# Optimization experiments

Hardware: AMD Instinct MI355X
Metric: run time of the kernel (lower is better)

## Reference

```python
import jax, jax.numpy as jnp
import numpy as np

B, S, D, V = 4, 1024, 512, 32000
INNER, NHM, DHM, QB = 1024, 4, 256, 4   # mLSTM: proj_factor 2.0 -> inner=2*D, 4 heads
NHS, DHS, K = 4, 128, 3                  # sLSTM: 4 heads over D, causal conv k=3
EPS = 1e-5


def layernorm(x, w):
    mu = x.mean(-1, keepdims=True)
    var = ((x - mu) ** 2).mean(-1, keepdims=True)
    return (x - mu) * jax.lax.rsqrt(var + EPS) * w


def headnorm(x, w):
    # x: (B,S,NH,DH) normalize per head over DH (GroupNorm), scale by w (NH*DH,)
    mu = x.mean(-1, keepdims=True)
    var = ((x - mu) ** 2).mean(-1, keepdims=True)
    xn = (x - mu) * jax.lax.rsqrt(var + EPS)
    b, s, nh, dh = x.shape
    return xn.reshape(b, s, nh * dh) * w


def causal_conv(x, w, bias):
    # depthwise causal conv: x (B,S,C), kernel w (C,K)
    k = w.shape[1]
    s = x.shape[1]
    xp = jnp.pad(x, ((0, 0), (k - 1, 0), (0, 0)))
    y = sum(xp[:, i:i + s, :] * w[:, i] for i in range(k))
    return y + bias


def blockdiag(x, w):
    # LinearHeadwiseExpand: block-diagonal linear, w (NB, out_bs, in_bs)
    b, s, _ = x.shape
    nb, ob, ib = w.shape
    return jnp.einsum('bsni,noi->bsno', x.reshape(b, s, nb, ib), w).reshape(b, s, nb * ob)


def mlstm_parallel(q, k, v, ig, fg):
    # parallel_stabilized_simple; q,k,v (B,NH,S,DH), ig/fg (B,NH,S)
    dh = q.shape[-1]
    s = q.shape[2]
    lf = jax.nn.log_sigmoid(fg)
    cs = jnp.cumsum(lf, axis=-1)
    logfmat = cs[..., :, None] - cs[..., None, :]      # (i,j) = sum_{j+1..i} log f
    mask = jnp.tril(jnp.ones((s, s), dtype=bool))
    logD = jnp.where(mask, logfmat + ig[..., None, :], -jnp.inf)
    maxD = logD.max(-1, keepdims=True)                 # rowwise stabilizer
    Dm = jnp.exp(logD - maxD)
    C = jnp.einsum('bhid,bhjd->bhij', q, k) * (dh ** -0.5) * Dm
    norm = jnp.maximum(jnp.abs(C.sum(-1, keepdims=True)), jnp.exp(-maxD))
    return jnp.einsum('bhij,bhjd->bhid', C / (norm + 1e-6), v)


def mlstm_block(x, p):
    (ln, Wup, convW, convb, Wq, Wk, Wv, Wi, bi, Wf, bf, skip, onorm, Wdown) = p
    b, s, _ = x.shape
    xin = layernorm(x, ln) @ Wup                        # (B,S,2*INNER)
    xm, z = jnp.split(xin, 2, axis=-1)
    xc = jax.nn.silu(causal_conv(xm, convW, convb))
    q = blockdiag(xc, Wq)
    kk = blockdiag(xc, Wk)
    v = blockdiag(xm, Wv)
    qkv = jnp.concatenate([q, kk, v], axis=-1)
    ig = (qkv @ Wi + bi).transpose(0, 2, 1)             # (B,NH,S)
    fg = (qkv @ Wf + bf).transpose(0, 2, 1)
    qh = q.reshape(b, s, NHM, DHM).transpose(0, 2, 1, 3)
    kh = kk.reshape(b, s, NHM, DHM).transpose(0, 2, 1, 3)
    vh = v.reshape(b, s, NHM, DHM).transpose(0, 2, 1, 3)
    h = mlstm_parallel(qh, kh, vh, ig, fg)              # (B,NH,S,DH)
    h = headnorm(h.transpose(0, 2, 1, 3), onorm)        # (B,S,INNER)
    h = (h + skip * xc) * jax.nn.silu(z)
    return x + h @ Wdown


def slstm_block(x, p):
    (ln1, convW, convb, Wig, Wfg, Wzg, Wog, R, bias, gn, ln2, Wu, Wd) = p
    b, s, _ = x.shape
    xn = layernorm(x, ln1)
    xc = jax.nn.silu(causal_conv(xn, convW, convb))

    def gate(inp, W):  # headwise linear, W (NH, DH, DH)
        return jnp.einsum('bshi,hoi->bsho', inp.reshape(b, s, NHS, DHS), W)

    # gate preactivations, gate order i,f,z,o: (B,S,4,NH,DH)
    Wx = jnp.stack([gate(xc, Wig), gate(xc, Wfg), gate(xn, Wzg), gate(xn, Wog)], axis=2)

    def step(carry, wx):
        y, c, n, m = carry
        raw = wx + jnp.einsum('bhd,hdge->bghe', y, R) + bias
        ir, fr, zr, orr = raw[:, 0], raw[:, 1], raw[:, 2], raw[:, 3]
        lfm = m + jax.nn.log_sigmoid(fr)
        mn = jnp.maximum(ir, lfm)                        # exp-gating stabilizer
        igt = jnp.exp(ir - mn)
        fgt = jnp.exp(lfm - mn)
        cn = fgt * c + igt * jnp.tanh(zr)
        nn_ = fgt * n + igt
        yn = jax.nn.sigmoid(orr) * cn / nn_
        return (yn, cn, nn_, mn), yn

    z0 = jnp.zeros((b, NHS, DHS), x.dtype)
    _, ys = jax.lax.scan(step, (z0, z0, z0, z0), Wx.transpose(1, 0, 2, 3, 4))
    h = x + headnorm(ys.transpose(1, 0, 2, 3), gn)
    # gated feedforward (proj_factor=1.0, gelu)
    u = layernorm(h, ln2) @ Wu
    g, up = jnp.split(u, 2, axis=-1)
    return h + (jax.nn.gelu(g, approximate=False) * up) @ Wd


def forward(x, emb, m0, s1, m2, post_ln, clf_W, clf_b):
    h = emb[x]
    h = mlstm_block(h, m0)
    h = slstm_block(h, s1)
    h = mlstm_block(h, m2)
    h = layernorm(h, post_ln)
    return h[:, -1, :] @ clf_W + clf_b


def setup_inputs() -> dict:
    key = jax.random.key(0)
    ks = iter(jax.random.split(key, 64))

    def rn(shape, s=0.02):
        return jax.random.normal(next(ks), shape, jnp.float32) * s

    def mblock():
        return dict(
            ln=jnp.ones((D,)), Wup=rn((D, 2 * INNER)),
            convW=rn((INNER, K), 0.1), convb=jnp.zeros((INNER,)),
            Wq=rn((INNER // QB, QB, QB), 0.2), Wk=rn((INNER // QB, QB, QB), 0.2),
            Wv=rn((INNER // QB, QB, QB), 0.2),
            Wi=rn((3 * INNER, NHM)), bi=rn((NHM,), 0.1),
            Wf=rn((3 * INNER, NHM)), bf=jnp.linspace(3.0, 6.0, NHM),
            skip=jnp.ones((INNER,)), onorm=jnp.ones((INNER,)), Wdown=rn((INNER, D)))

    m0 = mblock()
    m2 = mblock()
    emb = rn((V, D), 1.0).at[0].set(0.0)  # padding_idx=0 row zeroed
    inp = {'x': jax.random.randint(next(ks), (B, S), 0, V), 'emb': emb}
    for pre, m in (('m0_', m0), ('m2_', m2)):
        for k_, v_ in m.items():
            inp[pre + k_] = v_
    zb = jnp.zeros((NHS, DHS))
    inp.update(
        s1_ln1=jnp.ones((D,)), s1_convW=rn((D, K), 0.1), s1_convb=jnp.zeros((D,)),
        s1_Wig=rn((NHS, DHS, DHS), 0.1), s1_Wfg=rn((NHS, DHS, DHS), 0.1),
        s1_Wzg=rn((NHS, DHS, DHS), 0.1), s1_Wog=rn((NHS, DHS, DHS), 0.1),
        s1_R=rn((NHS, DHS, 4, DHS), 0.05),
        s1_b=jnp.stack([zb, jnp.linspace(3.0, 6.0, NHS)[:, None] * jnp.ones((NHS, DHS)), zb, zb], axis=0),
        s1_gn=jnp.ones((D,)), s1_ln2=jnp.ones((D,)),
        s1_Wu=rn((D, 2 * D)), s1_Wd=rn((D, D)),
        post_ln=jnp.ones((D,)), clf_W=rn((D, 1)), clf_b=jnp.zeros((1,)))
    return inp


def reference(x, emb, m0_ln, m0_Wup, m0_convW, m0_convb, m0_Wq, m0_Wk, m0_Wv, m0_Wi, m0_bi, m0_Wf, m0_bf, m0_skip, m0_onorm, m0_Wdown,
              s1_ln1, s1_convW, s1_convb, s1_Wig, s1_Wfg, s1_Wzg, s1_Wog, s1_R, s1_b, s1_gn, s1_ln2, s1_Wu, s1_Wd,
              m2_ln, m2_Wup, m2_convW, m2_convb, m2_Wq, m2_Wk, m2_Wv, m2_Wi, m2_bi, m2_Wf, m2_bf, m2_skip, m2_onorm, m2_Wdown,
              post_ln, clf_W, clf_b):
    m0 = (m0_ln, m0_Wup, m0_convW, m0_convb, m0_Wq, m0_Wk, m0_Wv, m0_Wi, m0_bi, m0_Wf, m0_bf, m0_skip, m0_onorm, m0_Wdown)
    s1 = (s1_ln1, s1_convW, s1_convb, s1_Wig, s1_Wfg, s1_Wzg, s1_Wog, s1_R, s1_b, s1_gn, s1_ln2, s1_Wu, s1_Wd)
    m2 = (m2_ln, m2_Wup, m2_convW, m2_convb, m2_Wq, m2_Wk, m2_Wv, m2_Wi, m2_bi, m2_Wf, m2_bf, m2_skip, m2_onorm, m2_Wdown)
    return forward(x, emb, m0, s1, m2, post_ln, clf_W, clf_b)
```

## Files before the change

### kernel.cpp

```cpp
#include <hip/hip_runtime.h>
#include <cstddef>
#include <cstdint>

#define EPSV 1e-5f

typedef __attribute__((ext_vector_type(8))) short bf16x8;
typedef __attribute__((ext_vector_type(4))) float f32x4;

__device__ __forceinline__ short f2bf(float f) {
  union { float f; unsigned u; } v; v.f = f;
  unsigned r = (v.u + 0x7FFFu + ((v.u >> 16) & 1u)) >> 16;
  return (short)r;
}
__device__ __forceinline__ float bf2f(short s) {
  union { unsigned u; float f; } v; v.u = ((unsigned)(unsigned short)s) << 16;
  return v.f;
}

__device__ __forceinline__ float wsum(float v) {
  v += __shfl_xor(v, 32, 64);
  v += __shfl_xor(v, 16, 64);
  v += __shfl_xor(v, 8, 64);
  v += __shfl_xor(v, 4, 64);
  v += __shfl_xor(v, 2, 64);
  v += __shfl_xor(v, 1, 64);
  return v;
}

__global__ __launch_bounds__(128) void k_embed(const int* __restrict__ x,
                                               const float* __restrict__ emb,
                                               float* __restrict__ out) {
  int t = blockIdx.x, tid = threadIdx.x;
  int row = x[t];
  const float4 v = *reinterpret_cast<const float4*>(emb + (size_t)row * 512 + tid * 4);
  *reinterpret_cast<float4*>(out + (size_t)t * 512 + tid * 4) = v;
}

__global__ __launch_bounds__(128) void k_ln512(const float* __restrict__ in,
                                               const float* __restrict__ w,
                                               float* __restrict__ outf,
                                               short* __restrict__ out16) {
  int t = blockIdx.x, tid = threadIdx.x;
  const float4 v = *reinterpret_cast<const float4*>(in + (size_t)t * 512 + tid * 4);
  float s = v.x + v.y + v.z + v.w;
  float s2 = v.x * v.x + v.y * v.y + v.z * v.z + v.w * v.w;
  s = wsum(s); s2 = wsum(s2);
  __shared__ float l1[2], l2[2];
  int wv = tid >> 6;
  if ((tid & 63) == 0) { l1[wv] = s; l2[wv] = s2; }
  __syncthreads();
  s = l1[0] + l1[1]; s2 = l2[0] + l2[1];
  float mu = s * (1.f / 512.f);
  float var = s2 * (1.f / 512.f) - mu * mu;
  float r = rsqrtf(var + EPSV);
  const float4 w4 = *reinterpret_cast<const float4*>(w + tid * 4);
  float4 o;
  o.x = (v.x - mu) * r * w4.x;
  o.y = (v.y - mu) * r * w4.y;
  o.z = (v.z - mu) * r * w4.z;
  o.w = (v.w - mu) * r * w4.w;
  if (outf) *reinterpret_cast<float4*>(outf + (size_t)t * 512 + tid * 4) = o;
  *reinterpret_cast<short4*>(out16 + (size_t)t * 512 + tid * 4) =
      make_short4(f2bf(o.x), f2bf(o.y), f2bf(o.z), f2bf(o.w));
}

template <bool OUT16, bool RES>
__global__ __launch_bounds__(256) void k_mm(
    const short* __restrict__ A, size_t sA1, size_t sA2, int lda,
    const short* __restrict__ B, size_t sB1, size_t sB2, int ldb,
    const float* __restrict__ Res, size_t sR1, size_t sR2, int ldr,
    void* __restrict__ Cv, size_t sC1, size_t sC2, int ldc,
    int K, int HB) {
  const int z = blockIdx.z, zh = z / HB, zl = z - zh * HB;
  A += zh * sA1 + zl * sA2;
  B += zh * sB1 + zl * sB2;
  const int bm = blockIdx.y * 128, bn = blockIdx.x * 128;
  const int tid = threadIdx.x, lane = tid & 63, w = tid >> 6;
  const int wr = w >> 1, wc = w & 1;
  const int l15 = lane & 15, l4 = lane >> 4;
  __shared__ short As[128 * 72];
  __shared__ short Bs[128 * 72];
  f32x4 acc[4][4];
#pragma unroll
  for (int i = 0; i < 4; ++i)
#pragma unroll
    for (int j = 0; j < 4; ++j) acc[i][j] = (f32x4){0.f, 0.f, 0.f, 0.f};
  const int srow = tid >> 3, sg = tid & 7;
  for (int k0 = 0; k0 < K; k0 += 64) {
    int4 ra[4], rb[4];
#pragma unroll
    for (int it = 0; it < 4; ++it) {
      int row = it * 32 + srow;
      ra[it] = *reinterpret_cast<const int4*>(A + (size_t)(bm + row) * lda + k0 + sg * 8);
      rb[it] = *reinterpret_cast<const int4*>(B + (size_t)(bn + row) * ldb + k0 + sg * 8);
    }
    __syncthreads();
#pragma unroll
    for (int it = 0; it < 4; ++it) {
      int row = it * 32 + srow;
      *reinterpret_cast<int4*>(As + row * 72 + sg * 8) = ra[it];
      *reinterpret_cast<int4*>(Bs + row * 72 + sg * 8) = rb[it];
    }
    __syncthreads();
#pragma unroll
    for (int kk = 0; kk < 2; ++kk) {
      bf16x8 af[4], bfr[4];
#pragma unroll
      for (int i = 0; i < 4; ++i) {
        af[i]  = *reinterpret_cast<const bf16x8*>(As + (wr * 64 + i * 16 + l15) * 72 + kk * 32 + l4 * 8);
        bfr[i] = *reinterpret_cast<const bf16x8*>(Bs + (wc * 64 + i * 16 + l15) * 72 + kk * 32 + l4 * 8);
      }
#pragma unroll
      for (int i = 0; i < 4; ++i)
#pragma unroll
        for (int j = 0; j < 4; ++j)
          acc[i][j] = __builtin_amdgcn_mfma_f32_16x16x32_bf16(af[i], bfr[j], acc[i][j], 0, 0, 0);
    }
  }
  const int row0 = bm + wr * 64 + l4 * 4, col0 = bn + wc * 64 + l15;
  if constexpr (OUT16) {
    short* C = (short*)Cv + zh * sC1 + zl * sC2;
#pragma unroll
    for (int mi = 0; mi < 4; ++mi)
#pragma unroll
      for (int r = 0; r < 4; ++r) {
        size_t ro = (size_t)(row0 + mi * 16 + r) * ldc;
#pragma unroll
        for (int ni = 0; ni < 4; ++ni) C[ro + col0 + ni * 16] = f2bf(acc[mi][ni][r]);
      }
  } else {
    float* C = (float*)Cv + zh * sC1 + zl * sC2;
    const float* Rp = Res ? (Res + zh * sR1 + zl * sR2) : nullptr;
#pragma unroll
    for (int mi = 0; mi < 4; ++mi)
#pragma unroll
      for (int r = 0; r < 4; ++r) {
        int rw = row0 + mi * 16 + r;
#pragma unroll
        for (int ni = 0; ni < 4; ++ni) {
          float vv = acc[mi][ni][r];
          if constexpr (RES) vv += Rp[(size_t)rw * ldr + col0 + ni * 16];
          C[(size_t)rw * ldc + col0 + ni * 16] = vv;
        }
      }
  }
}

__global__ __launch_bounds__(256) void k_transp(const float* __restrict__ in, size_t sI1, size_t sI2, int ldi,
                                                short* __restrict__ out, size_t sO1, size_t sO2, int ldo,
                                                int HB) {
  __shared__ float t[32][33];
  int z = blockIdx.z, zh = z / HB, zl = z - zh * HB;
  in += zh * sI1 + zl * sI2;
  out += zh * sO1 + zl * sO2;
  int r0 = blockIdx.x * 32, c0 = blockIdx.y * 32;
  int tx = threadIdx.x & 31, ty = threadIdx.x >> 5;
#pragma unroll
  for (int i = 0; i < 4; ++i) {
    int rr = ty + i * 8;
    t[rr][tx] = in[(size_t)(r0 + rr) * ldi + c0 + tx];
  }
  __syncthreads();
#pragma unroll
  for (int i = 0; i < 4; ++i) {
    int cr = ty + i * 8;
    out[(size_t)(c0 + cr) * ldo + r0 + tx] = f2bf(t[tx][cr]);
  }
}

__global__ __launch_bounds__(256) void k_conv_silu(const float* __restrict__ in, int inLd, int logC,
                                                   const float* __restrict__ w,
                                                   const float* __restrict__ bias,
                                                   float* __restrict__ out,
                                                   short* __restrict__ out16) {
  int idx = blockIdx.x * 256 + threadIdx.x;
  int C = 1 << logC;
  int t = idx >> logC, c = idx & (C - 1);
  int s = t & 1023;
  const float* ip = in + (size_t)t * inLd + c;
  float acc = bias[c] + w[c * 3 + 2] * ip[0];
  if (s >= 1) acc += w[c * 3 + 1] * ip[-(ptrdiff_t)inLd];
  if (s >= 2) acc += w[c * 3 + 0] * ip[-2 * (ptrdiff_t)inLd];
  float r = acc / (1.f + __expf(-acc));
  out[(size_t)t * C + c] = r;
  if (out16) out16[(size_t)t * C + c] = f2bf(r);
}

__global__ __launch_bounds__(256) void k_qkv(const float* __restrict__ xc, const float* __restrict__ x2,
                                             const float* __restrict__ Wq, const float* __restrict__ Wk,
                                             const float* __restrict__ Wv,
                                             float* __restrict__ q, float* __restrict__ k,
                                             float* __restrict__ v,
                                             short* __restrict__ q16, short* __restrict__ k16) {
  int t = blockIdx.x, n = threadIdx.x;
  const float4 xcv = *reinterpret_cast<const float4*>(xc + (size_t)t * 1024 + n * 4);
  const float4 xmv = *reinterpret_cast<const float4*>(x2 + (size_t)t * 2048 + n * 4);
  float qa[4], ka[4], va[4];
#pragma unroll
  for (int o = 0; o < 4; ++o) {
    const float4 wq = *reinterpret_cast<const float4*>(Wq + n * 16 + o * 4);
    const float4 wk = *reinterpret_cast<const float4*>(Wk + n * 16 + o * 4);
    const float4 wv = *reinterpret_cast<const float4*>(Wv + n * 16 + o * 4);
    qa[o] = xcv.x * wq.x + xcv.y * wq.y + xcv.z * wq.z + xcv.w * wq.w;
    ka[o] = xcv.x * wk.x + xcv.y * wk.y + xcv.z * wk.z + xcv.w * wk.w;
    va[o] = xmv.x * wv.x + xmv.y * wv.y + xmv.z * wv.z + xmv.w * wv.w;
  }
  *reinterpret_cast<float4*>(q + (size_t)t * 1024 + n * 4) = make_float4(qa[0], qa[1], qa[2], qa[3]);
  *reinterpret_cast<float4*>(k + (size_t)t * 1024 + n * 4) = make_float4(ka[0], ka[1], ka[2], ka[3]);
  *reinterpret_cast<float4*>(v + (size_t)t * 1024 + n * 4) = make_float4(va[0], va[1], va[2], va[3]);
  *reinterpret_cast<short4*>(q16 + (size_t)t * 1024 + n * 4) =
      make_short4(f2bf(qa[0]), f2bf(qa[1]), f2bf(qa[2]), f2bf(qa[3]));
  *reinterpret_cast<short4*>(k16 + (size_t)t * 1024 + n * 4) =
      make_short4(f2bf(ka[0]), f2bf(ka[1]), f2bf(ka[2]), f2bf(ka[3]));
}

__global__ __launch_bounds__(256) void k_igfg(const float* __restrict__ q, const float* __restrict__ k,
                                              const float* __restrict__ v,
                                              const float* __restrict__ Wi, const float* __restrict__ bi,
                                              const float* __restrict__ Wf, const float* __restrict__ bf,
                                              float* __restrict__ ig, float* __restrict__ fg) {
  int t = blockIdx.x, tid = threadIdx.x;
  float aI[4] = {0.f, 0.f, 0.f, 0.f}, aF[4] = {0.f, 0.f, 0.f, 0.f};
  for (int c = tid; c < 1024; c += 256) {
    float qv = q[(size_t)t * 1024 + c];
    float kv = k[(size_t)t * 1024 + c];
    float vv = v[(size_t)t * 1024 + c];
    const float4 wiq = *reinterpret_cast<const float4*>(Wi + (size_t)c * 4);
    const float4 wik = *reinterpret_cast<const float4*>(Wi + (size_t)(1024 + c) * 4);
    const float4 wiv = *reinterpret_cast<const float4*>(Wi + (size_t)(2048 + c) * 4);
    const float4 wfq = *reinterpret_cast<const float4*>(Wf + (size_t)c * 4);
    const float4 wfk = *reinterpret_cast<const float4*>(Wf + (size_t)(1024 + c) * 4);
    const float4 wfv = *reinterpret_cast<const float4*>(Wf + (size_t)(2048 + c) * 4);
    aI[0] += qv * wiq.x + kv * wik.x + vv * wiv.x;
    aI[1] += qv * wiq.y + kv * wik.y + vv * wiv.y;
    aI[2] += qv * wiq.z + kv * wik.z + vv * wiv.z;
    aI[3] += qv * wiq.w + kv * wik.w + vv * wiv.w;
    aF[0] += qv * wfq.x + kv * wfk.x + vv * wfv.x;
    aF[1] += qv * wfq.y + kv * wfk.y + vv * wfv.y;
    aF[2] += qv * wfq.z + kv * wfk.z + vv * wfv.z;
    aF[3] += qv * wfq.w + kv * wfk.w + vv * wfv.w;
  }
#pragma unroll
  for (int h = 0; h < 4; ++h) { aI[h] = wsum(aI[h]); aF[h] = wsum(aF[h]); }
  __shared__ float red[2][4][4];
  int wv = tid >> 6;
  if ((tid & 63) == 0) {
#pragma unroll
    for (int h = 0; h < 4; ++h) { red[0][wv][h] = aI[h]; red[1][wv][h] = aF[h]; }
  }
  __syncthreads();
  if (tid < 8) {
    int which = tid >> 2, h = tid & 3;
    float sum = red[which][0][h] + red[which][1][h] + red[which][2][h] + red[which][3][h];
    int b = t >> 10, s = t & 1023;
    size_t o = (size_t)(b * 4 + h) * 1024 + s;
    if (which == 0) ig[o] = sum + bi[h];
    else            fg[o] = sum + bf[h];
  }
}

__global__ __launch_bounds__(1024) void k_gatescan(const float* __restrict__ ig, const float* __restrict__ fg,
                                                   float* __restrict__ a, float* __restrict__ Mx,
                                                   float* __restrict__ emax) {
  int bh = blockIdx.x, s = threadIdx.x;
  size_t o = (size_t)bh * 1024 + s;
  float f = fg[o];
  float lf = (f >= 0.f) ? -log1pf(__expf(-f)) : (f - log1pf(__expf(f)));
  __shared__ float buf[1024];
  float val = lf;
  buf[s] = val;
  __syncthreads();
#pragma unroll
  for (int off = 1; off < 1024; off <<= 1) {
    float add = (s >= off) ? buf[s - off] : 0.f;
    __syncthreads();
    val += add; buf[s] = val;
    __syncthreads();
  }
  float csv = val;
  float av = ig[o] - csv;
  float mv = av;
  buf[s] = mv;
  __syncthreads();
#pragma unroll
  for (int off = 1; off < 1024; off <<= 1) {
    float other = (s >= off) ? buf[s - off] : -3.4e38f;
    __syncthreads();
    mv = fmaxf(mv, other); buf[s] = mv;
    __syncthreads();
  }
  a[o] = av;
  Mx[o] = mv;
  emax[o] = __expf(-(csv + mv));
}

__global__ __launch_bounds__(256) void k_mask(short* __restrict__ P, const float* __restrict__ a,
                                              const float* __restrict__ Mx, const float* __restrict__ emax,
                                              int bhBase) {
  int i = blockIdx.x, z = blockIdx.y, tid = threadIdx.x;
  int bh = bhBase + z;
  short* Prow = P + ((size_t)z * 1024 + i) * 1024;
  const float* ab = a + (size_t)bh * 1024;
  float Mi = Mx[(size_t)bh * 1024 + i];
  float vals[4];
  float rs = 0.f;
#pragma unroll
  for (int jj = 0; jj < 4; ++jj) {
    int j = tid + jj * 256;
    float pv = 0.f;
    if (j <= i) pv = bf2f(Prow[j]) * 0.0625f * __expf(ab[j] - Mi);
    vals[jj] = pv;
    rs += pv;
  }
  rs = wsum(rs);
  __shared__ float red[4];
  if ((tid & 63) == 0) red[tid >> 6] = rs;
  __syncthreads();
  float tot = red[0] + red[1] + red[2] + red[3];
  float norm = fmaxf(fabsf(tot), emax[(size_t)bh * 1024 + i]) + 1e-6f;
  float inv = 1.f / norm;
#pragma unroll
  for (int jj = 0; jj < 4; ++jj) Prow[tid + jj * 256] = f2bf(vals[jj] * inv);
}

__global__ __launch_bounds__(256) void k_hncomb(const float* __restrict__ hattn, const float* __restrict__ xc,
                                                const float* __restrict__ x2, const float* __restrict__ onorm,
                                                const float* __restrict__ skip, short* __restrict__ out) {
  int t = blockIdx.x, tid = threadIdx.x;
  int w = tid >> 6, lane = tid & 63;
  int cbase = w * 256 + lane * 4;
  const float4 v = *reinterpret_cast<const float4*>(hattn + (size_t)t * 1024 + cbase);
  float s = v.x + v.y + v.z + v.w;
  float s2 = v.x * v.x + v.y * v.y + v.z * v.z + v.w * v.w;
  s = wsum(s); s2 = wsum(s2);
  float mu = s * (1.f / 256.f), var = s2 * (1.f / 256.f) - mu * mu;
  float r = rsqrtf(var + EPSV);
  const float4 on4 = *reinterpret_cast<const float4*>(onorm + cbase);
  const float4 sk4 = *reinterpret_cast<const float4*>(skip + cbase);
  const float4 xc4 = *reinterpret_cast<const float4*>(xc + (size_t)t * 1024 + cbase);
  const float4 z4 = *reinterpret_cast<const float4*>(x2 + (size_t)t * 2048 + 1024 + cbase);
  float4 o;
  o.x = ((v.x - mu) * r * on4.x + sk4.x * xc4.x) * (z4.x / (1.f + __expf(-z4.x)));
  o.y = ((v.y - mu) * r * on4.y + sk4.y * xc4.y) * (z4.y / (1.f + __expf(-z4.y)));
  o.z = ((v.z - mu) * r * on4.z + sk4.z * xc4.z) * (z4.z / (1.f + __expf(-z4.z)));
  o.w = ((v.w - mu) * r * on4.w + sk4.w * xc4.w) * (z4.w / (1.f + __expf(-z4.w)));
  *reinterpret_cast<short4*>(out + (size_t)t * 1024 + cbase) =
      make_short4(f2bf(o.x), f2bf(o.y), f2bf(o.z), f2bf(o.w));
}

__global__ __launch_bounds__(256) void k_wcat(const float* __restrict__ wi, const float* __restrict__ wf,
                                              const float* __restrict__ wz, const float* __restrict__ wo,
                                              short* __restrict__ Wcat) {
  int idx = blockIdx.x * 256 + threadIdx.x;
  int g = idx >> 16, r = idx & 65535;
  const float* s = (g == 0) ? wi : ((g == 1) ? wf : ((g == 2) ? wz : wo));
  Wcat[idx] = f2bf(s[r]);
}

__global__ __launch_bounds__(512, 2) void k_scan(const float* __restrict__ Wx, const float* __restrict__ R,
                                                 const float* __restrict__ bias, float* __restrict__ ys) {
  int bh = blockIdx.x, b = bh >> 2, h = bh & 3;
  int tid = threadIdx.x;
  int dg = tid >> 7, oq = tid & 127;
  float rr[32][4];
  {
    const float* Rp = R + (size_t)h * 65536 + (size_t)(dg * 32) * 512 + oq * 4;
#pragma unroll
    for (int d2 = 0; d2 < 32; ++d2) {
      const float4 rv = *reinterpret_cast<const float4*>(Rp + (size_t)d2 * 512);
      rr[d2][0] = rv.x; rr[d2][1] = rv.y; rr[d2][2] = rv.z; rr[d2][3] = rv.w;
    }
  }
  __shared__ float ysh[128];
  __shared__ float part[4][512];
  float c_ = 0.f, n_ = 0.f, m_ = 0.f;
  float bsv[4] = {0.f, 0.f, 0.f, 0.f}, wx[4] = {0.f, 0.f, 0.f, 0.f};
  const float* wxp = Wx;
  if (tid < 128) {
    int e = tid;
#pragma unroll
    for (int g = 0; g < 4; ++g) bsv[g] = bias[(size_t)g * 512 + h * 128 + e];
    wxp = Wx + (size_t)b * 1024 * 2048 + h * 512 + e;
#pragma unroll
    for (int g = 0; g < 4; ++g) wx[g] = wxp[g * 128];
    ysh[e] = 0.f;
  }
  __syncthreads();
  for (int s = 0; s < 1024; ++s) {
    float a0 = 0.f, a1 = 0.f, a2 = 0.f, a3 = 0.f;
    const float* yp = ysh + dg * 32;
#pragma unroll
    for (int c4 = 0; c4 < 8; ++c4) {
      const float4 yv = *reinterpret_cast<const float4*>(yp + c4 * 4);
      a0 = fmaf(yv.x, rr[c4 * 4 + 0][0], a0); a1 = fmaf(yv.x, rr[c4 * 4 + 0][1], a1);
      a2 = fmaf(yv.x, rr[c4 * 4 + 0][2], a2); a3 = fmaf(yv.x, rr[c4 * 4 + 0][3], a3);
      a0 = fmaf(yv.y, rr[c4 * 4 + 1][0], a0); a1 = fmaf(yv.y, rr[c4 * 4 + 1][1], a1);
      a2 = fmaf(yv.y, rr[c4 * 4 + 1][2], a2); a3 = fmaf(yv.y, rr[c4 * 4 + 1][3], a3);
      a0 = fmaf(yv.z, rr[c4 * 4 + 2][0], a0); a1 = fmaf(yv.z, rr[c4 * 4 + 2][1], a1);
      a2 = fmaf(yv.z, rr[c4 * 4 + 2][2], a2); a3 = fmaf(yv.z, rr[c4 * 4 + 2][3], a3);
      a0 = fmaf(yv.w, rr[c4 * 4 + 3][0], a0); a1 = fmaf(yv.w, rr[c4 * 4 + 3][1], a1);
      a2 = fmaf(yv.w, rr[c4 * 4 + 3][2], a2); a3 = fmaf(yv.w, rr[c4 * 4 + 3][3], a3);
    }
    *reinterpret_cast<float4*>(&part[dg][oq * 4]) = make_float4(a0, a1, a2, a3);
    __syncthreads();
    if (tid < 128) {
      int e = tid;
      float raw[4];
#pragma unroll
      for (int g = 0; g < 4; ++g)
        raw[g] = wx[g] + bsv[g] +
                 ((part[0][g * 128 + e] + part[1][g * 128 + e]) +
                  (part[2][g * 128 + e] + part[3][g * 128 + e]));
      int sp = (s + 1 < 1024) ? (s + 1) : 1023;
#pragma unroll
      for (int g = 0; g < 4; ++g) wx[g] = wxp[(size_t)sp * 2048 + g * 128];
      float fr = raw[1];
      float lsf = (fr >= 0.f) ? -log1pf(__expf(-fr)) : (fr - log1pf(__expf(fr)));
      float lfm = m_ + lsf;
      float mn = fmaxf(raw[0], lfm);
      float igt = __expf(raw[0] - mn);
      float fgt = __expf(lfm - mn);
      float cn = fgt * c_ + igt * tanhf(raw[2]);
      float nn = fgt * n_ + igt;
      float yn = (1.f / (1.f + __expf(-raw[3]))) * cn / nn;
      c_ = cn; n_ = nn; m_ = mn;
      ysh[e] = yn;
      ys[((size_t)b * 1024 + s) * 512 + h * 128 + e] = yn;
    }
    __syncthreads();
  }
}

__global__ __launch_bounds__(512) void k_hnadd(const float* __restrict__ hin, const float* __restrict__ ysv,
                                               const float* __restrict__ gn, float* __restrict__ out) {
  int t = blockIdx.x, tid = threadIdx.x;
  float yv = ysv[(size_t)t * 512 + tid];
  float s = wsum(yv), s2 = wsum(yv * yv);
  __shared__ float l1[8], l2[8];
  int wv = tid >> 6;
  if ((tid & 63) == 0) { l1[wv] = s; l2[wv] = s2; }
  __syncthreads();
  int h2 = (tid >> 7) * 2;
  float S = l1[h2] + l1[h2 + 1], S2 = l2[h2] + l2[h2 + 1];
  float mu = S * (1.f / 128.f), var = S2 * (1.f / 128.f) - mu * mu;
  float r = rsqrtf(var + EPSV);
  out[(size_t)t * 512 + tid] = hin[(size_t)t * 512 + tid] + (yv - mu) * r * gn[tid];
}

__global__ __launch_bounds__(256) void k_geluprod(const float* __restrict__ u, short* __restrict__ gp) {
  int idx = blockIdx.x * 256 + threadIdx.x;
  int t = idx >> 9, c = idx & 511;
  float g = u[(size_t)t * 1024 + c];
  float up = u[(size_t)t * 1024 + 512 + c];
  float ge = 0.5f * g * (1.f + erff(g * 0.70710678118654752f));
  gp[idx] = f2bf(ge * up);
}

__global__ __launch_bounds__(128) void k_final(const float* __restrict__ h, const float* __restrict__ w,
                                               const float* __restrict__ cw, const float* __restrict__ cb,
                                               float* __restrict__ out) {
  int b = blockIdx.x, tid = threadIdx.x;
  const float* row = h + ((size_t)(b * 1024 + 1023)) * 512;
  const float4 v = *reinterpret_cast<const float4*>(row + tid * 4);
  float s = v.x + v.y + v.z + v.w;
  float s2 = v.x * v.x + v.y * v.y + v.z * v.z + v.w * v.w;
  s = wsum(s); s2 = wsum(s2);
  __shared__ float l1[2], l2[2];
  int wv = tid >> 6;
  if ((tid & 63) == 0) { l1[wv] = s; l2[wv] = s2; }
  __syncthreads();
  s = l1[0] + l1[1]; s2 = l2[0] + l2[1];
  float mu = s * (1.f / 512.f);
  float var = s2 * (1.f / 512.f) - mu * mu;
  float r = rsqrtf(var + EPSV);
  const float4 w4 = *reinterpret_cast<const float4*>(w + tid * 4);
  const float4 c4 = *reinterpret_cast<const float4*>(cw + tid * 4);
  float d = (v.x - mu) * r * w4.x * c4.x + (v.y - mu) * r * w4.y * c4.y +
            (v.z - mu) * r * w4.z * c4.z + (v.w - mu) * r * w4.w * c4.w;
  d = wsum(d);
  __syncthreads();
  if ((tid & 63) == 0) l1[tid >> 6] = d;
  __syncthreads();
  if (tid == 0) out[b] = l1[0] + l1[1] + cb[0];
}

extern "C" void kernel_launch(void* const* d_in, const int* in_sizes, int n_in,
                              void* d_out, int out_size, void* d_ws, size_t ws_size,
                              hipStream_t stream) {
  (void)in_sizes; (void)n_in; (void)out_size; (void)ws_size;
  auto F = [&](int i) { return (const float*)d_in[i]; };
  const int* x = (const int*)d_in[0];
  const float* emb = F(1);

  float* ws = (float*)d_ws;
  size_t off = 0;
  auto alloc = [&](size_t n) { float* p = ws + off; off += n; return p; };
  float* hA = alloc(2097152);
  float* hB = alloc(2097152);
  float* X2 = alloc(8388608);
  float* C1 = alloc(4194304);
  float* C2 = alloc(4194304);
  float* C3 = alloc(4194304);
  float* C4 = alloc(4194304);
  float* C5 = alloc(4194304);
  float* g_a = alloc(16384);
  float* g_M = alloc(16384);
  float* g_e = alloc(16384);
  float* g_ig = alloc(16384);
  float* g_fg = alloc(16384);
  short* q16 = (short*)alloc(2097152);
  short* k16 = (short*)alloc(2097152);
  short* A16a = (short*)alloc(1048576);
  short* A16b = (short*)alloc(1048576);
  short* WT = (short*)alloc(524288);
  short* Wc16 = (short*)alloc(131072);
  short* Pb16 = (short*)C2;
  short* VT = (short*)C3;
  short* H16 = (short*)q16;

  k_embed<<<4096, 128, 0, stream>>>(x, emb, hA);

  auto mlstm = [&](int pi, const float* hin, float* hout) {
    const float* ln = F(pi);       const float* Wup = F(pi + 1);
    const float* convW = F(pi + 2); const float* convb = F(pi + 3);
    const float* Wq = F(pi + 4);   const float* Wk = F(pi + 5);  const float* Wv = F(pi + 6);
    const float* Wi = F(pi + 7);   const float* bi = F(pi + 8);
    const float* Wf = F(pi + 9);   const float* bf_ = F(pi + 10);
    const float* skip = F(pi + 11); const float* onorm = F(pi + 12);
    const float* Wdown = F(pi + 13);

    k_ln512<<<4096, 128, 0, stream>>>(hin, ln, nullptr, A16a);
    k_transp<<<dim3(16, 64, 1), 256, 0, stream>>>(Wup, 0, 0, 2048, WT, 0, 0, 512, 1);
    k_mm<false, false><<<dim3(16, 32, 1), 256, 0, stream>>>(
        A16a, 0, 0, 512, WT, 0, 0, 512, nullptr, 0, 0, 0, X2, 0, 0, 2048, 512, 1);
    k_conv_silu<<<(4096 * 1024) / 256, 256, 0, stream>>>(X2, 2048, 10, convW, convb, C1, nullptr);
    k_qkv<<<4096, 256, 0, stream>>>(C1, X2, Wq, Wk, Wv, C2, C3, C4, q16, k16);
    k_igfg<<<4096, 256, 0, stream>>>(C2, C3, C4, Wi, bi, Wf, bf_, g_ig, g_fg);
    k_gatescan<<<16, 1024, 0, stream>>>(g_ig, g_fg, g_a, g_M, g_e);
    k_transp<<<dim3(32, 8, 16), 256, 0, stream>>>(C4, 1048576, 256, 1024, VT, 1048576, 262144, 1024, 4);
    for (int c = 0; c < 2; ++c) {
      const short* qc = q16 + (size_t)c * 2097152;
      const short* kc = k16 + (size_t)c * 2097152;
      k_mm<true, false><<<dim3(8, 8, 8), 256, 0, stream>>>(
          qc, 1048576, 256, 1024, kc, 1048576, 256, 1024,
          nullptr, 0, 0, 0, Pb16, 4194304, 1048576, 1024, 256, 4);
      k_mask<<<dim3(1024, 8), 256, 0, stream>>>(Pb16, g_a, g_M, g_e, c * 8);
      k_mm<false, false><<<dim3(2, 8, 8), 256, 0, stream>>>(
          Pb16, 4194304, 1048576, 1024, VT + (size_t)c * 8 * 262144, 1048576, 262144, 1024,
          nullptr, 0, 0, 0, C5 + (size_t)c * 2097152, 1048576, 256, 1024, 1024, 4);
    }
    k_hncomb<<<4096, 256, 0, stream>>>(C5, C1, X2, onorm, skip, H16);
    k_transp<<<dim3(32, 16, 1), 256, 0, stream>>>(Wdown, 0, 0, 512, WT, 0, 0, 1024, 1);
    k_mm<false, true><<<dim3(4, 32, 1), 256, 0, stream>>>(
        H16, 0, 0, 1024, WT, 0, 0, 1024, hin, 0, 0, 512, hout, 0, 0, 512, 1024, 1);
  };

  auto slstm = [&](const float* hin, float* hout) {
    const float* ln1 = F(30); const float* convW = F(31); const float* convb = F(32);
    const float* Wig = F(33); const float* Wfg = F(34); const float* Wzg = F(35);
    const float* Wog = F(36); const float* Rr = F(37);  const float* bias = F(38);
    const float* gn = F(39);  const float* ln2 = F(40);
    const float* Wu = F(41);  const float* Wd = F(42);

    k_ln512<<<4096, 128, 0, stream>>>(hin, ln1, C3, A16a);
    k_conv_silu<<<(4096 * 512) / 256, 256, 0, stream>>>(C3, 512, 9, convW, convb, C4, A16b);
    k_wcat<<<(4 * 65536) / 256, 256, 0, stream>>>(Wig, Wfg, Wzg, Wog, Wc16);
    k_mm<false, false><<<dim3(1, 32, 8), 256, 0, stream>>>(
        A16b, 128, 0, 512, Wc16, 16384, 65536, 128,
        nullptr, 0, 0, 0, X2, 512, 128, 2048, 128, 2);
    k_mm<false, false><<<dim3(1, 32, 8), 256, 0, stream>>>(
        A16a, 128, 0, 512, Wc16 + 131072, 16384, 65536, 128,
        nullptr, 0, 0, 0, X2 + 256, 512, 128, 2048, 128, 2);
    k_scan<<<16, 512, 0, stream>>>(X2, Rr, bias, C2);
    k_hnadd<<<4096, 512, 0, stream>>>(hin, C2, gn, C3);
    k_ln512<<<4096, 128, 0, stream>>>(C3, ln2, nullptr, A16a);
    k_transp<<<dim3(16, 32, 1), 256, 0, stream>>>(Wu, 0, 0, 1024, WT, 0, 0, 512, 1);
    k_mm<false, false><<<dim3(8, 32, 1), 256, 0, stream>>>(
        A16a, 0, 0, 512, WT, 0, 0, 512, nullptr, 0, 0, 0, C5, 0, 0, 1024, 512, 1);
    k_geluprod<<<(4096 * 512) / 256, 256, 0, stream>>>(C5, A16b);
    k_transp<<<dim3(16, 16, 1), 256, 0, stream>>>(Wd, 0, 0, 512, WT, 0, 0, 512, 1);
    k_mm<false, true><<<dim3(4, 32, 1), 256, 0, stream>>>(
        A16b, 0, 0, 512, WT, 0, 0, 512, C3, 0, 0, 512, hout, 0, 0, 512, 512, 1);
  };

  mlstm(2, hA, hB);
  slstm(hB, hA);
  mlstm(16, hA, hB);
  k_final<<<4, 128, 0, stream>>>(hB, F(43), F(44), F(45), (float*)d_out);
}
```

Measured before the change: 2.074 ms.

## Restructure sLSTM scan so each thread owns a full gate row, one barrier per step

The recurrent scan kernel is reorganized so each of the 512 threads computes one full 128-long dot product for a single (unit, gate) pair. The four gate values are exchanged with wavefront shuffles instead of a shared-memory partial-sum reduction, and the y state is double-buffered so each timestep needs only one __syncthreads instead of two. Gate math also switches to fast __logf/__expf approximations, including a manual tanh. The cost is 128 recurrent weights per thread in registers (occupancy bound lowered to 1 block per CU) and a small loss of transcendental accuracy.

```diff
diff --git a/kernel.cpp b/kernel.cpp
--- a/kernel.cpp
+++ b/kernel.cpp
@@ -6,6 +6,7 @@
 
 typedef __attribute__((ext_vector_type(8))) short bf16x8;
 typedef __attribute__((ext_vector_type(4))) float f32x4;
+typedef __attribute__((ext_vector_type(2))) float f32x2;
 
 __device__ __forceinline__ short f2bf(float f) {
   union { float f; unsigned u; } v; v.f = f;
@@ -357,76 +358,66 @@
   Wcat[idx] = f2bf(s[r]);
 }
 
-__global__ __launch_bounds__(512, 2) void k_scan(const float* __restrict__ Wx, const float* __restrict__ R,
+__global__ __launch_bounds__(512, 1) void k_scan(const float* __restrict__ Wx, const float* __restrict__ R,
                                                  const float* __restrict__ bias, float* __restrict__ ys) {
   int bh = blockIdx.x, b = bh >> 2, h = bh & 3;
   int tid = threadIdx.x;
-  int dg = tid >> 7, oq = tid & 127;
-  float rr[32][4];
+  int e = tid >> 2, g = tid & 3;
+  f32x2 rc[64];
   {
-    const float* Rp = R + (size_t)h * 65536 + (size_t)(dg * 32) * 512 + oq * 4;
-#pragma unroll
-    for (int d2 = 0; d2 < 32; ++d2) {
-      const float4 rv = *reinterpret_cast<const float4*>(Rp + (size_t)d2 * 512);
-      rr[d2][0] = rv.x; rr[d2][1] = rv.y; rr[d2][2] = rv.z; rr[d2][3] = rv.w;
-    }
-  }
-  __shared__ float ysh[128];
-  __shared__ float part[4][512];
+    const float* Rp = R + (size_t)h * 65536 + g * 128 + e;
+#pragma unroll
+    for (int i = 0; i < 64; ++i) {
+      rc[i][0] = Rp[(size_t)(2 * i) * 512];
+      rc[i][1] = Rp[(size_t)(2 * i + 1) * 512];
+    }
+  }
+  const float bsv = bias[(size_t)g * 512 + h * 128 + e];
+  const float* wxp = Wx + (size_t)b * 1024 * 2048 + h * 512 + g * 128 + e;
+  __shared__ float ysh[2][128];
+  if (tid < 128) { ysh[0][tid] = 0.f; ysh[1][tid] = 0.f; }
   float c_ = 0.f, n_ = 0.f, m_ = 0.f;
-  float bsv[4] = {0.f, 0.f, 0.f, 0.f}, wx[4] = {0.f, 0.f, 0.f, 0.f};
-  const float* wxp = Wx;
-  if (tid < 128) {
-    int e = tid;
-#pragma unroll
-    for (int g = 0; g < 4; ++g) bsv[g] = bias[(size_t)g * 512 + h * 128 + e];
-    wxp = Wx + (size_t)b * 1024 * 2048 + h * 512 + e;
-#pragma unroll
-    for (int g = 0; g < 4; ++g) wx[g] = wxp[g * 128];
-    ysh[e] = 0.f;
-  }
+  float wx = wxp[0];
+  float* ysg = ys + ((size_t)b * 1024) * 512 + h * 128 + e;
   __syncthreads();
   for (int s = 0; s < 1024; ++s) {
-    float a0 = 0.f, a1 = 0.f, a2 = 0.f, a3 = 0.f;
-    const float* yp = ysh + dg * 32;
-#pragma unroll
-    for (int c4 = 0; c4 < 8; ++c4) {
-      const float4 yv = *reinterpret_cast<const float4*>(yp + c4 * 4);
-      a0 = fmaf(yv.x, rr[c4 * 4 + 0][0], a0); a1 = fmaf(yv.x, rr[c4 * 4 + 0][1], a1);
-      a2 = fmaf(yv.x, rr[c4 * 4 + 0][2], a2); a3 = fmaf(yv.x, rr[c4 * 4 + 0][3], a3);
-      a0 = fmaf(yv.y, rr[c4 * 4 + 1][0], a0); a1 = fmaf(yv.y, rr[c4 * 4 + 1][1], a1);
-      a2 = fmaf(yv.y, rr[c4 * 4 + 1][2], a2); a3 = fmaf(yv.y, rr[c4 * 4 + 1][3], a3);
-      a0 = fmaf(yv.z, rr[c4 * 4 + 2][0], a0); a1 = fmaf(yv.z, rr[c4 * 4 + 2][1], a1);
-      a2 = fmaf(yv.z, rr[c4 * 4 + 2][2], a2); a3 = fmaf(yv.z, rr[c4 * 4 + 2][3], a3);
-      a0 = fmaf(yv.w, rr[c4 * 4 + 3][0], a0); a1 = fmaf(yv.w, rr[c4 * 4 + 3][1], a1);
-      a2 = fmaf(yv.w, rr[c4 * 4 + 3][2], a2); a3 = fmaf(yv.w, rr[c4 * 4 + 3][3], a3);
-    }
-    *reinterpret_cast<float4*>(&part[dg][oq * 4]) = make_float4(a0, a1, a2, a3);
-    __syncthreads();
-    if (tid < 128) {
-      int e = tid;
-      float raw[4];
-#pragma unroll
-      for (int g = 0; g < 4; ++g)
-        raw[g] = wx[g] + bsv[g] +
-                 ((part[0][g * 128 + e] + part[1][g * 128 + e]) +
-                  (part[2][g * 128 + e] + part[3][g * 128 + e]));
-      int sp = (s + 1 < 1024) ? (s + 1) : 1023;
-#pragma unroll
-      for (int g = 0; g < 4; ++g) wx[g] = wxp[(size_t)sp * 2048 + g * 128];
-      float fr = raw[1];
-      float lsf = (fr >= 0.f) ? -log1pf(__expf(-fr)) : (fr - log1pf(__expf(fr)));
-      float lfm = m_ + lsf;
-      float mn = fmaxf(raw[0], lfm);
-      float igt = __expf(raw[0] - mn);
-      float fgt = __expf(lfm - mn);
-      float cn = fgt * c_ + igt * tanhf(raw[2]);
-      float nn = fgt * n_ + igt;
-      float yn = (1.f / (1.f + __expf(-raw[3]))) * cn / nn;
-      c_ = cn; n_ = nn; m_ = mn;
-      ysh[e] = yn;
-      ys[((size_t)b * 1024 + s) * 512 + h * 128 + e] = yn;
-    }
+    const float* yb = &ysh[(s + 1) & 1][0];
+    int sp = (s + 1 < 1024) ? (s + 1) : 1023;
+    float wxn = wxp[(size_t)sp * 2048];
+    f32x2 accA = {0.f, 0.f}, accB = {0.f, 0.f};
+#pragma unroll
+    for (int i = 0; i < 32; ++i) {
+      const f32x2 y0 = *reinterpret_cast<const f32x2*>(yb + i * 4);
+      const f32x2 y1 = *reinterpret_cast<const f32x2*>(yb + i * 4 + 2);
+      accA = y0 * rc[2 * i] + accA;
+      accB = y1 * rc[2 * i + 1] + accB;
+    }
+    float raw = ((accA[0] + accB[0]) + (accA[1] + accB[1])) + wx + bsv;
+    float o1 = __shfl_xor(raw, 1, 64);
+    float o2 = __shfl_xor(raw, 2, 64);
+    float o3 = __shfl_xor(o1, 2, 64);
+    const bool g0 = (g & 1) != 0, g1 = (g & 2) != 0;
+    float ir  = g1 ? (g0 ? o3 : o2) : (g0 ? o1 : raw);
+    float fr  = g1 ? (g0 ? o2 : o3) : (g0 ? raw : o1);
+    float zr  = g1 ? (g0 ? o1 : raw) : (g0 ? o3 : o2);
+    float orr = g1 ? (g0 ? raw : o1) : (g0 ? o2 : o3);
+    float lsf = (fr >= 0.f) ? -__logf(1.f + __expf(-fr)) : (fr - __logf(1.f + __expf(fr)));
+    float lfm = m_ + lsf;
+    float mn = fmaxf(ir, lfm);
+    float igt = __expf(ir - mn);
+    float fgt = __expf(lfm - mn);
+    float t2 = __expf(-2.f * fabsf(zr));
+    float th = (1.f - t2) / (1.f + t2);
+    th = (zr >= 0.f) ? th : -th;
+    float cn = fgt * c_ + igt * th;
+    float nn = fgt * n_ + igt;
+    float yn = cn / (nn * (1.f + __expf(-orr)));
+    c_ = cn; n_ = nn; m_ = mn;
+    if (g == 0) {
+      ysh[s & 1][e] = yn;
+      ysg[(size_t)s * 512] = yn;
+    }
+    wx = wxn;
     __syncthreads();
   }
 }
```

New measurement: 1.943 ms. 6.3% less time.
